# Performance work log

Measured on AMD Instinct MI355X. Metric: run time of the kernel, lower is better.

Reference implementation:

```python
import jax, jax.numpy as jnp
import numpy as np

# ---- static module config (matches init_kwargs) ----
N = 16384
E_DIM = 256
SHARE_N_E = 2048
SPECIFIC = [1024, 1024, 1024]
TOTAL_N_E = SHARE_N_E + sum(SPECIFIC)  # 5120
BETA = 0.25
NUM_MOD = len(SPECIFIC)
BIG = 1e7  # value written into masked-out distance entries

# prefix boundaries of the per-modality code blocks: [2048, 3072, 4096, 5120]
CODE_BOUNDS = jnp.asarray(np.cumsum([SHARE_N_E] + SPECIFIC)[:, None].squeeze(-1) if False else np.cumsum([SHARE_N_E] + SPECIFIC), dtype=jnp.int32)
# code -> modality id; shared codes get -1
CODE_MOD = jnp.searchsorted(CODE_BOUNDS, jnp.arange(TOTAL_N_E, dtype=jnp.int32), side='right') - 1  # [TOTAL_N_E]


def setup_inputs() -> dict:
    key = jax.random.key(0)
    k1, k2 = jax.random.split(key)
    x = jax.random.normal(k1, (N, E_DIM), dtype=jnp.float32)
    emb_weight = jax.random.normal(k2, (TOTAL_N_E, E_DIM), dtype=jnp.float32)  # nn.Embedding default N(0,1)
    split_index = jnp.array([0, 5120, 10240, 16384], dtype=jnp.int64)  # 3 equal modality segments
    return {"x": x, "emb_weight": emb_weight, "split_index": split_index}


def reference(x, emb_weight, split_index):
    # pairwise squared distances d[n, c] = ||x_n||^2 + ||e_c||^2 - 2 x_n . e_c
    d = (jnp.sum(x * x, axis=1, keepdims=True)
         + jnp.sum(emb_weight * emb_weight, axis=1)[None, :]
         - 2.0 * jnp.einsum('nd,cd->nc', x, emb_weight))  # [N, TOTAL_N_E]

    # token -> modality id via split boundaries (vectorized form of the Python loop)
    tok_mod = jnp.searchsorted(split_index, jnp.arange(N, dtype=split_index.dtype), side='right') - 1  # [N]
    tok_mod = tok_mod.astype(jnp.int32)
    # allowed = shared code OR code's modality matches token's modality
    allowed = (CODE_MOD[None, :] == -1) | (CODE_MOD[None, :] == tok_mod[:, None])  # [N, TOTAL_N_E]
    d = jnp.where(allowed, d, jnp.float32(BIG))

    indices = jnp.argmin(d, axis=-1)              # [N]
    x_q = jnp.take(emb_weight, indices, axis=0)   # [N, E_DIM]

    # per-modality VQ losses: codebook + beta * commitment (mse over segment)
    sg = jax.lax.stop_gradient
    se_commit = jnp.sum((sg(x_q) - x) ** 2, axis=1)   # [N]
    se_code = jnp.sum((x_q - sg(x)) ** 2, axis=1)     # [N]
    seg_commit = jax.ops.segment_sum(se_commit, tok_mod, num_segments=NUM_MOD)
    seg_code = jax.ops.segment_sum(se_code, tok_mod, num_segments=NUM_MOD)
    counts = (split_index[1:] - split_index[:-1]).astype(jnp.float32) * jnp.float32(E_DIM)
    q_losses = seg_code / counts + BETA * (seg_commit / counts)  # [NUM_MOD]

    # straight-through estimator
    x_q_ste = x + sg(x_q - x)
    return (x_q_ste, indices, d, q_losses)
```

## Files before the change

kernel.cpp:

```cpp
#include <hip/hip_runtime.h>
#include <stdint.h>

#define N_TOK    16384
#define E_DIM    256
#define N_CODE   5120
#define N_SHARED 2048
#define BIGF     1e7f

#define BM  128
#define BN  128
#define BK  32
#define NCB (N_CODE / BN)
#define NKC (E_DIM / BK)
#define CHUNK (BM * BK)

#define IDX_OFF ((size_t)N_TOK * E_DIM)
#define D_OFF   (IDX_OFF + N_TOK)
#define QL_OFF  (D_OFF + (size_t)N_TOK * N_CODE)

typedef float f32x4 __attribute__((ext_vector_type(4)));
typedef short bf16x8 __attribute__((ext_vector_type(8)));
typedef short s16x4 __attribute__((ext_vector_type(4)));

typedef __attribute__((address_space(1))) const unsigned int g_u32;
typedef __attribute__((address_space(3))) unsigned int lds_u32;

__device__ __forceinline__ unsigned short bf16_rn(float f) {
    unsigned u = __float_as_uint(f);
    u += 0x7FFF + ((u >> 16) & 1);
    return (unsigned short)(u >> 16);
}
__device__ __forceinline__ float bf16_to_f(unsigned short h) {
    return __uint_as_float(((unsigned)h) << 16);
}

__global__ __launch_bounds__(256) void convert_kernel(const float* __restrict__ x,
                                                      const float* __restrict__ emb,
                                                      float* __restrict__ xx,
                                                      float* __restrict__ ee,
                                                      short* __restrict__ xhi, short* __restrict__ xlo,
                                                      short* __restrict__ ehi, short* __restrict__ elo) {
    int wid = threadIdx.x >> 6, ln = threadIdx.x & 63;
    int row = blockIdx.x * 4 + wid;
    const float* src; float* nrm; short *hiA, *loA; int rl, tb;
    if (row < N_TOK) {
        src = x + (size_t)row * E_DIM; nrm = xx + row;
        tb = row >> 7; rl = row & 127; hiA = xhi; loA = xlo;
    } else {
        int r = row - N_TOK;
        src = emb + (size_t)r * E_DIM; nrm = ee + r;
        tb = r >> 7; rl = r & 127; hiA = ehi; loA = elo;
    }
    f32x4 v = ((const f32x4*)src)[ln];
    float s = v[0]*v[0] + v[1]*v[1] + v[2]*v[2] + v[3]*v[3];
    s16x4 h, l;
#pragma unroll
    for (int c = 0; c < 4; ++c) {
        unsigned short hh = bf16_rn(v[c]);
        h[c] = (short)hh;
        l[c] = (short)bf16_rn(v[c] - bf16_to_f(hh));
    }
    int kc = ln >> 3, q = (ln >> 1) & 3, kl4 = (ln & 1) * 4;
    size_t di = ((((size_t)tb * NKC + kc) * 4 + q) * BM + rl) * 8 + kl4;
    *(s16x4*)&hiA[di] = h;
    *(s16x4*)&loA[di] = l;
#pragma unroll
    for (int sh = 32; sh; sh >>= 1) s += __shfl_xor(s, sh, 64);
    if (ln == 0) *nrm = s;
}

__global__ __launch_bounds__(256, 2) void gemm_kernel(const short* __restrict__ xhi,
                                                      const short* __restrict__ xlo,
                                                      const short* __restrict__ ehi,
                                                      const short* __restrict__ elo,
                                                      const int* __restrict__ split,
                                                      const float* __restrict__ xx,
                                                      const float* __restrict__ ee,
                                                      float* __restrict__ out) {
    __shared__ short Ah[CHUNK], Al[CHUNK], Bh[CHUNK], Bl[CHUNK];
    __shared__ float xxs[BM];
    __shared__ float ees[BN];
    __shared__ float redv[2][BM];
    __shared__ int   redi[2][BM];

    const int bx = blockIdx.x;
    const int by = blockIdx.y;
    const int m0 = by * BM, n0 = bx * BN;
    const int t = threadIdx.x;

    const int s1 = split[1], s2v = split[2];
    const int tmFirst = (m0 >= s1) + (m0 >= s2v);
    const int tmLast  = ((m0 + BM - 1) >= s1) + ((m0 + BM - 1) >= s2v);
    const bool rowUni = (tmFirst == tmLast);
    const int cmod = (n0 < N_SHARED) ? -1 : ((n0 - N_SHARED) >> 10);

    float* dOut = out + D_OFF;
    float* pmin = out;
    int*   pidx = (int*)(out + (size_t)N_TOK * NCB);

    if (cmod >= 0 && rowUni && cmod != tmFirst) {
        int row = t >> 1, ch = t & 1;
        f32x4* p = (f32x4*)(dOut + (size_t)(m0 + row) * N_CODE + n0 + ch * 64);
        f32x4 big = {BIGF, BIGF, BIGF, BIGF};
#pragma unroll
        for (int u = 0; u < 16; ++u) p[u] = big;
        if (t < BM) {
            pmin[(size_t)(m0 + t) * NCB + bx] = BIGF;
            pidx[(size_t)(m0 + t) * NCB + bx] = n0;
        }
        return;
    }

    const bool allAllowed = (cmod < 0) || (rowUni && cmod == tmFirst);

    if (t < BM) xxs[t] = xx[m0 + t];
    else        ees[t - BM] = ee[n0 + (t - BM)];

    f32x4 acc[4][4] = {};

    const int wid = t >> 6, lane = t & 63;
    const int quad = lane >> 4, ln16 = lane & 15;
    const int wr = (wid >> 1) * 64, wc = (wid & 1) * 64;

    const short* aHiG = xhi + (size_t)by * NKC * CHUNK;
    const short* aLoG = xlo + (size_t)by * NKC * CHUNK;
    const short* bHiG = ehi + (size_t)bx * NKC * CHUNK;
    const short* bLoG = elo + (size_t)bx * NKC * CHUNK;
    const int tOff = t * 8;

    for (int kc = 0; kc < NKC; ++kc) {
        __syncthreads();
        const int co = kc * CHUNK;
#pragma unroll
        for (int p = 0; p < 2; ++p) {
            int o = p * 2048 + tOff;
            __builtin_amdgcn_global_load_lds((g_u32*)(aHiG + co + o), (lds_u32*)&Ah[o], 16, 0, 0);
            __builtin_amdgcn_global_load_lds((g_u32*)(aLoG + co + o), (lds_u32*)&Al[o], 16, 0, 0);
            __builtin_amdgcn_global_load_lds((g_u32*)(bHiG + co + o), (lds_u32*)&Bh[o], 16, 0, 0);
            __builtin_amdgcn_global_load_lds((g_u32*)(bLoG + co + o), (lds_u32*)&Bl[o], 16, 0, 0);
        }
        __syncthreads();

        bf16x8 ah[4], al[4], bh[4], bl[4];
#pragma unroll
        for (int i = 0; i < 4; ++i) {
            int a = (quad * BM + wr + i * 16 + ln16) * 8;
            ah[i] = *(const bf16x8*)&Ah[a];
            al[i] = *(const bf16x8*)&Al[a];
        }
#pragma unroll
        for (int j = 0; j < 4; ++j) {
            int b = (quad * BM + wc + j * 16 + ln16) * 8;
            bh[j] = *(const bf16x8*)&Bh[b];
            bl[j] = *(const bf16x8*)&Bl[b];
        }
#pragma unroll
        for (int i = 0; i < 4; ++i)
#pragma unroll
            for (int j = 0; j < 4; ++j) {
                acc[i][j] = __builtin_amdgcn_mfma_f32_16x16x32_bf16(ah[i], bh[j], acc[i][j], 0, 0, 0);
                acc[i][j] = __builtin_amdgcn_mfma_f32_16x16x32_bf16(ah[i], bl[j], acc[i][j], 0, 0, 0);
                acc[i][j] = __builtin_amdgcn_mfma_f32_16x16x32_bf16(al[i], bh[j], acc[i][j], 0, 0, 0);
            }
    }

#pragma unroll
    for (int i = 0; i < 4; ++i) {
#pragma unroll
        for (int r = 0; r < 4; ++r) {
            int lm = wr + i * 16 + quad * 4 + r;
            int gm = m0 + lm;
            float xv = xxs[lm];
            int tmod = (gm >= s1) + (gm >= s2v);
            float best = 3.4e38f;
            int bidx = n0;
#pragma unroll
            for (int j = 0; j < 4; ++j) {
                int lnn = wc + j * 16 + ln16;
                int gn = n0 + lnn;
                float dv = fmaf(-2.f, acc[i][j][r], xv + ees[lnn]);
                if (!allAllowed) {
                    bool ok = (gn < N_SHARED) || (((gn - N_SHARED) >> 10) == tmod);
                    if (!ok) dv = BIGF;
                }
                dOut[(size_t)gm * N_CODE + gn] = dv;
                if (dv < best) { best = dv; bidx = gn; }
            }
#pragma unroll
            for (int s = 1; s < 16; s <<= 1) {
                float ov = __shfl_xor(best, s, 64);
                int   oi = __shfl_xor(bidx, s, 64);
                if (ov < best || (ov == best && oi < bidx)) { best = ov; bidx = oi; }
            }
            if (ln16 == 0) { redv[wid & 1][lm] = best; redi[wid & 1][lm] = bidx; }
        }
    }
    __syncthreads();
    if (t < BM) {
        float v0 = redv[0][t]; int i0 = redi[0][t];
        float v1 = redv[1][t]; int i1 = redi[1][t];
        if (v1 < v0 || (v1 == v0 && i1 < i0)) { v0 = v1; i0 = i1; }
        pmin[(size_t)(m0 + t) * NCB + bx] = v0;
        pidx[(size_t)(m0 + t) * NCB + bx] = i0;
    }
}

__global__ __launch_bounds__(256) void reduce_kernel(float* __restrict__ out) {
    int tk = blockIdx.x * 256 + threadIdx.x;
    const float* pmin = out;
    const int* pidx = (const int*)(out + (size_t)N_TOK * NCB);
    float best = pmin[(size_t)tk * NCB];
    int bi = pidx[(size_t)tk * NCB];
    for (int j = 1; j < NCB; ++j) {
        float v = pmin[(size_t)tk * NCB + j];
        int ii = pidx[(size_t)tk * NCB + j];
        if (v < best || (v == best && ii < bi)) { best = v; bi = ii; }
    }
    out[IDX_OFF + tk] = (float)bi;
}

__global__ __launch_bounds__(256) void gather_kernel(const float* __restrict__ x,
                                                     const float* __restrict__ emb,
                                                     const int* __restrict__ split,
                                                     float* __restrict__ out,
                                                     float* __restrict__ wsLoss) {
    __shared__ float ls[3];
    int t = threadIdx.x, wid = t >> 6, ln = t & 63;
    if (t < 3) ls[t] = 0.f;
    __syncthreads();
    int tok = blockIdx.x * 4 + wid;
    int idx = (int)out[IDX_OFF + tok];
    f32x4 e  = ((const f32x4*)(emb + (size_t)idx * E_DIM))[ln];
    f32x4 xv = ((const f32x4*)(x + (size_t)tok * E_DIM))[ln];
    f32x4 q;
    float s = 0.f;
#pragma unroll
    for (int c = 0; c < 4; ++c) {
        float d = e[c] - xv[c];
        q[c] = xv[c] + d;
        s = fmaf(d, d, s);
    }
    ((f32x4*)(out + (size_t)tok * E_DIM))[ln] = q;
#pragma unroll
    for (int sh = 32; sh; sh >>= 1) s += __shfl_xor(s, sh, 64);
    if (ln == 0) {
        int mod = (tok >= split[1]) + (tok >= split[2]);
        atomicAdd(&ls[mod], s);
    }
    __syncthreads();
    if (t < 3) wsLoss[blockIdx.x * 3 + t] = ls[t];
}

__global__ __launch_bounds__(256) void loss_kernel(const float* __restrict__ wsLoss,
                                                   const int* __restrict__ split,
                                                   float* __restrict__ out, int nblk) {
    __shared__ float red[256];
    float s[3] = {0.f, 0.f, 0.f};
    for (int b = threadIdx.x; b < nblk; b += 256) {
        s[0] += wsLoss[b * 3 + 0];
        s[1] += wsLoss[b * 3 + 1];
        s[2] += wsLoss[b * 3 + 2];
    }
    for (int m = 0; m < 3; ++m) {
        red[threadIdx.x] = s[m];
        __syncthreads();
        for (int st = 128; st; st >>= 1) {
            if (threadIdx.x < st) red[threadIdx.x] += red[threadIdx.x + st];
            __syncthreads();
        }
        if (threadIdx.x == 0) {
            float cnt = (float)(split[m + 1] - split[m]) * (float)E_DIM;
            float a = red[0] / cnt;
            out[QL_OFF + m] = a + 0.25f * a;
        }
        __syncthreads();
    }
}

extern "C" void kernel_launch(void* const* d_in, const int* in_sizes, int n_in,
                              void* d_out, int out_size, void* d_ws, size_t ws_size,
                              hipStream_t stream) {
    const float* x   = (const float*)d_in[0];
    const float* emb = (const float*)d_in[1];
    const int* split = (const int*)d_in[2];
    float* out = (float*)d_out;

    float* xx     = (float*)d_ws;
    float* ee     = xx + N_TOK;
    float* wsLoss = ee + N_CODE;
    short* xhi    = (short*)(wsLoss + 4096 * 3);
    short* xlo    = xhi + (size_t)N_TOK * E_DIM;
    short* ehi    = xlo + (size_t)N_TOK * E_DIM;
    short* elo    = ehi + (size_t)N_CODE * E_DIM;
    int nblkGather = N_TOK / 4;

    convert_kernel<<<dim3((N_TOK + N_CODE) / 4), dim3(256), 0, stream>>>(x, emb, xx, ee, xhi, xlo, ehi, elo);
    gemm_kernel<<<dim3(NCB, N_TOK / BM), dim3(256), 0, stream>>>(xhi, xlo, ehi, elo, split, xx, ee, out);
    reduce_kernel<<<dim3(N_TOK / 256), dim3(256), 0, stream>>>(out);
    gather_kernel<<<dim3(nblkGather), dim3(256), 0, stream>>>(x, emb, split, out, wsLoss);
    loss_kernel<<<dim3(1), dim3(256), 0, stream>>>(wsLoss, split, out, nblkGather);
}
```

Measured before the change: 485.6 us.

## Enlarge GEMM tiles to 256x256, double-buffer LDS, fuse argmin reduce into gather

Raises the distance GEMM tile from 128x128 to 256x256 with 512 threads and double-buffered LDS. Loads of the hi and lo bf16 halves are split into staggered stages with explicit vmcnt waits and raised MFMA priority, so global-to-LDS transfers overlap the three-pass split-bf16 MFMA. The partial argmin arrays move to workspace, and the standalone reduce kernel is folded into the gather kernel as a wave shuffle reduction. The costs are higher register pressure (32 accumulators per thread), more LDS use that may cut occupancy, and fewer blocks in the grid.

```diff
diff --git a/kernel.cpp b/kernel.cpp
--- a/kernel.cpp
+++ b/kernel.cpp
@@ -7,11 +7,11 @@
 #define N_SHARED 2048
 #define BIGF     1e7f
 
-#define BM  128
-#define BN  128
+#define BM  256
+#define BN  256
 #define BK  32
 #define NCB (N_CODE / BN)
-#define NKC (E_DIM / BK)
+#define NKT (E_DIM / BK)
 #define CHUNK (BM * BK)
 
 #define IDX_OFF ((size_t)N_TOK * E_DIM)
@@ -24,6 +24,8 @@
 
 typedef __attribute__((address_space(1))) const unsigned int g_u32;
 typedef __attribute__((address_space(3))) unsigned int lds_u32;
+
+#define VMW(n) asm volatile("s_waitcnt vmcnt(" #n ")" ::: "memory")
 
 __device__ __forceinline__ unsigned short bf16_rn(float f) {
     unsigned u = __float_as_uint(f);
@@ -45,11 +47,11 @@
     const float* src; float* nrm; short *hiA, *loA; int rl, tb;
     if (row < N_TOK) {
         src = x + (size_t)row * E_DIM; nrm = xx + row;
-        tb = row >> 7; rl = row & 127; hiA = xhi; loA = xlo;
+        tb = row >> 8; rl = row & 255; hiA = xhi; loA = xlo;
     } else {
         int r = row - N_TOK;
         src = emb + (size_t)r * E_DIM; nrm = ee + r;
-        tb = r >> 7; rl = r & 127; hiA = ehi; loA = elo;
+        tb = r >> 8; rl = r & 255; hiA = ehi; loA = elo;
     }
     f32x4 v = ((const f32x4*)src)[ln];
     float s = v[0]*v[0] + v[1]*v[1] + v[2]*v[2] + v[3]*v[3];
@@ -60,8 +62,8 @@
         h[c] = (short)hh;
         l[c] = (short)bf16_rn(v[c] - bf16_to_f(hh));
     }
-    int kc = ln >> 3, q = (ln >> 1) & 3, kl4 = (ln & 1) * 4;
-    size_t di = ((((size_t)tb * NKC + kc) * 4 + q) * BM + rl) * 8 + kl4;
+    int kt = ln >> 3, q = (ln >> 1) & 3, kl4 = (ln & 1) * 4;
+    size_t di = ((((size_t)tb * NKT + kt) * 4 + q) * BM + rl) * 8 + kl4;
     *(s16x4*)&hiA[di] = h;
     *(s16x4*)&loA[di] = l;
 #pragma unroll
@@ -69,19 +71,22 @@
     if (ln == 0) *nrm = s;
 }
 
-__global__ __launch_bounds__(256, 2) void gemm_kernel(const short* __restrict__ xhi,
+__global__ __launch_bounds__(512, 2) void gemm_kernel(const short* __restrict__ xhi,
                                                       const short* __restrict__ xlo,
                                                       const short* __restrict__ ehi,
                                                       const short* __restrict__ elo,
                                                       const int* __restrict__ split,
                                                       const float* __restrict__ xx,
                                                       const float* __restrict__ ee,
-                                                      float* __restrict__ out) {
-    __shared__ short Ah[CHUNK], Al[CHUNK], Bh[CHUNK], Bl[CHUNK];
+                                                      float* __restrict__ out,
+                                                      float* __restrict__ pmin,
+                                                      int*   __restrict__ pidx) {
+    __shared__ short Ah[2][CHUNK], Bh[2][CHUNK];
+    __shared__ short Al[2][CHUNK], Bl[2][CHUNK];
     __shared__ float xxs[BM];
     __shared__ float ees[BN];
-    __shared__ float redv[2][BM];
-    __shared__ int   redi[2][BM];
+    __shared__ float redv[4][BM];
+    __shared__ int   redi[4][BM];
 
     const int bx = blockIdx.x;
     const int by = blockIdx.y;
@@ -95,15 +100,13 @@
     const int cmod = (n0 < N_SHARED) ? -1 : ((n0 - N_SHARED) >> 10);
 
     float* dOut = out + D_OFF;
-    float* pmin = out;
-    int*   pidx = (int*)(out + (size_t)N_TOK * NCB);
 
     if (cmod >= 0 && rowUni && cmod != tmFirst) {
-        int row = t >> 1, ch = t & 1;
-        f32x4* p = (f32x4*)(dOut + (size_t)(m0 + row) * N_CODE + n0 + ch * 64);
+        int row = t >> 1, half = t & 1;
+        f32x4* p = (f32x4*)(dOut + (size_t)(m0 + row) * N_CODE + n0 + half * 128);
         f32x4 big = {BIGF, BIGF, BIGF, BIGF};
 #pragma unroll
-        for (int u = 0; u < 16; ++u) p[u] = big;
+        for (int u = 0; u < 32; ++u) p[u] = big;
         if (t < BM) {
             pmin[(size_t)(m0 + t) * NCB + bx] = BIGF;
             pidx[(size_t)(m0 + t) * NCB + bx] = n0;
@@ -115,57 +118,88 @@
 
     if (t < BM) xxs[t] = xx[m0 + t];
     else        ees[t - BM] = ee[n0 + (t - BM)];
-
-    f32x4 acc[4][4] = {};
+    __syncthreads();
+
+    f32x4 acc[8][4] = {};
 
     const int wid = t >> 6, lane = t & 63;
     const int quad = lane >> 4, ln16 = lane & 15;
-    const int wr = (wid >> 1) * 64, wc = (wid & 1) * 64;
-
-    const short* aHiG = xhi + (size_t)by * NKC * CHUNK;
-    const short* aLoG = xlo + (size_t)by * NKC * CHUNK;
-    const short* bHiG = ehi + (size_t)bx * NKC * CHUNK;
-    const short* bLoG = elo + (size_t)bx * NKC * CHUNK;
+    const int wr = (wid >> 2) * 128, wc = (wid & 3) * 64;
+    const int qb = quad * BM;
+
+    const short* aHiG = xhi + (size_t)by * NKT * CHUNK;
+    const short* aLoG = xlo + (size_t)by * NKT * CHUNK;
+    const short* bHiG = ehi + (size_t)bx * NKT * CHUNK;
+    const short* bLoG = elo + (size_t)bx * NKT * CHUNK;
     const int tOff = t * 8;
 
-    for (int kc = 0; kc < NKC; ++kc) {
-        __syncthreads();
-        const int co = kc * CHUNK;
+    auto stageU0 = [&](int kt, int b) {
+        const size_t co = (size_t)kt * CHUNK;
 #pragma unroll
         for (int p = 0; p < 2; ++p) {
-            int o = p * 2048 + tOff;
-            __builtin_amdgcn_global_load_lds((g_u32*)(aHiG + co + o), (lds_u32*)&Ah[o], 16, 0, 0);
-            __builtin_amdgcn_global_load_lds((g_u32*)(aLoG + co + o), (lds_u32*)&Al[o], 16, 0, 0);
-            __builtin_amdgcn_global_load_lds((g_u32*)(bHiG + co + o), (lds_u32*)&Bh[o], 16, 0, 0);
-            __builtin_amdgcn_global_load_lds((g_u32*)(bLoG + co + o), (lds_u32*)&Bl[o], 16, 0, 0);
-        }
-        __syncthreads();
-
-        bf16x8 ah[4], al[4], bh[4], bl[4];
-#pragma unroll
-        for (int i = 0; i < 4; ++i) {
-            int a = (quad * BM + wr + i * 16 + ln16) * 8;
-            ah[i] = *(const bf16x8*)&Ah[a];
-            al[i] = *(const bf16x8*)&Al[a];
-        }
-#pragma unroll
-        for (int j = 0; j < 4; ++j) {
-            int b = (quad * BM + wc + j * 16 + ln16) * 8;
-            bh[j] = *(const bf16x8*)&Bh[b];
-            bl[j] = *(const bf16x8*)&Bl[b];
-        }
-#pragma unroll
-        for (int i = 0; i < 4; ++i)
-#pragma unroll
-            for (int j = 0; j < 4; ++j) {
-                acc[i][j] = __builtin_amdgcn_mfma_f32_16x16x32_bf16(ah[i], bh[j], acc[i][j], 0, 0, 0);
-                acc[i][j] = __builtin_amdgcn_mfma_f32_16x16x32_bf16(ah[i], bl[j], acc[i][j], 0, 0, 0);
-                acc[i][j] = __builtin_amdgcn_mfma_f32_16x16x32_bf16(al[i], bh[j], acc[i][j], 0, 0, 0);
-            }
-    }
-
-#pragma unroll
-    for (int i = 0; i < 4; ++i) {
+            int o = p * 4096 + tOff;
+            __builtin_amdgcn_global_load_lds((g_u32*)(aHiG + co + o), (lds_u32*)&Ah[b][o], 16, 0, 0);
+            __builtin_amdgcn_global_load_lds((g_u32*)(bHiG + co + o), (lds_u32*)&Bh[b][o], 16, 0, 0);
+        }
+    };
+    auto stageU1 = [&](int kt, int b) {
+        const size_t co = (size_t)kt * CHUNK;
+#pragma unroll
+        for (int p = 0; p < 2; ++p) {
+            int o = p * 4096 + tOff;
+            __builtin_amdgcn_global_load_lds((g_u32*)(aLoG + co + o), (lds_u32*)&Al[b][o], 16, 0, 0);
+            __builtin_amdgcn_global_load_lds((g_u32*)(bLoG + co + o), (lds_u32*)&Bl[b][o], 16, 0, 0);
+        }
+    };
+
+    stageU0(0, 0); stageU1(0, 0); stageU0(1, 1);
+    int cur = 0;
+
+#define TILE(VA, VB, DOU1, DOU2, KT)                                                         \
+    {                                                                                        \
+        VMW(VA);                                                                             \
+        __builtin_amdgcn_s_barrier();                                                        \
+        if (DOU1) stageU1((KT) + 1, cur ^ 1);                                                \
+        bf16x8 ah[8], bh[4];                                                                 \
+        _Pragma("unroll") for (int i = 0; i < 8; ++i)                                        \
+            ah[i] = *(const bf16x8*)&Ah[cur][(qb + wr + i * 16 + ln16) * 8];                 \
+        _Pragma("unroll") for (int j = 0; j < 4; ++j)                                        \
+            bh[j] = *(const bf16x8*)&Bh[cur][(qb + wc + j * 16 + ln16) * 8];                 \
+        __builtin_amdgcn_s_setprio(1);                                                       \
+        _Pragma("unroll") for (int i = 0; i < 8; ++i)                                        \
+            _Pragma("unroll") for (int j = 0; j < 4; ++j)                                    \
+                acc[i][j] = __builtin_amdgcn_mfma_f32_16x16x32_bf16(ah[i], bh[j], acc[i][j], 0, 0, 0); \
+        __builtin_amdgcn_s_setprio(0);                                                       \
+        VMW(VB);                                                                             \
+        __builtin_amdgcn_s_barrier();                                                        \
+        if (DOU2) stageU0((KT) + 2, cur);                                                    \
+        bf16x8 bl[4];                                                                        \
+        _Pragma("unroll") for (int j = 0; j < 4; ++j)                                        \
+            bl[j] = *(const bf16x8*)&Bl[cur][(qb + wc + j * 16 + ln16) * 8];                 \
+        __builtin_amdgcn_s_setprio(1);                                                       \
+        _Pragma("unroll") for (int i = 0; i < 8; ++i)                                        \
+            _Pragma("unroll") for (int j = 0; j < 4; ++j)                                    \
+                acc[i][j] = __builtin_amdgcn_mfma_f32_16x16x32_bf16(ah[i], bl[j], acc[i][j], 0, 0, 0); \
+        __builtin_amdgcn_s_setprio(0);                                                       \
+        bf16x8 al[8];                                                                        \
+        _Pragma("unroll") for (int i = 0; i < 8; ++i)                                        \
+            al[i] = *(const bf16x8*)&Al[cur][(qb + wr + i * 16 + ln16) * 8];                 \
+        __builtin_amdgcn_s_setprio(1);                                                       \
+        _Pragma("unroll") for (int i = 0; i < 8; ++i)                                        \
+            _Pragma("unroll") for (int j = 0; j < 4; ++j)                                    \
+                acc[i][j] = __builtin_amdgcn_mfma_f32_16x16x32_bf16(al[i], bh[j], acc[i][j], 0, 0, 0); \
+        __builtin_amdgcn_s_setprio(0);                                                       \
+        cur ^= 1;                                                                            \
+    }
+
+    for (int kt = 0; kt < NKT - 2; ++kt)
+        TILE(8, 8, true, true, kt);
+    TILE(8, 8, true, false, NKT - 2);
+    TILE(4, 0, false, false, NKT - 1);
+#undef TILE
+
+#pragma unroll
+    for (int i = 0; i < 8; ++i) {
 #pragma unroll
         for (int r = 0; r < 4; ++r) {
             int lm = wr + i * 16 + quad * 4 + r;
@@ -192,44 +226,50 @@
                 int   oi = __shfl_xor(bidx, s, 64);
                 if (ov < best || (ov == best && oi < bidx)) { best = ov; bidx = oi; }
             }
-            if (ln16 == 0) { redv[wid & 1][lm] = best; redi[wid & 1][lm] = bidx; }
+            if (ln16 == 0) { redv[wid & 3][lm] = best; redi[wid & 3][lm] = bidx; }
         }
     }
     __syncthreads();
     if (t < BM) {
         float v0 = redv[0][t]; int i0 = redi[0][t];
-        float v1 = redv[1][t]; int i1 = redi[1][t];
-        if (v1 < v0 || (v1 == v0 && i1 < i0)) { v0 = v1; i0 = i1; }
+#pragma unroll
+        for (int w = 1; w < 4; ++w) {
+            float v = redv[w][t]; int ii = redi[w][t];
+            if (v < v0 || (v == v0 && ii < i0)) { v0 = v; i0 = ii; }
+        }
         pmin[(size_t)(m0 + t) * NCB + bx] = v0;
         pidx[(size_t)(m0 + t) * NCB + bx] = i0;
     }
-}
-
-__global__ __launch_bounds__(256) void reduce_kernel(float* __restrict__ out) {
-    int tk = blockIdx.x * 256 + threadIdx.x;
-    const float* pmin = out;
-    const int* pidx = (const int*)(out + (size_t)N_TOK * NCB);
-    float best = pmin[(size_t)tk * NCB];
-    int bi = pidx[(size_t)tk * NCB];
-    for (int j = 1; j < NCB; ++j) {
-        float v = pmin[(size_t)tk * NCB + j];
-        int ii = pidx[(size_t)tk * NCB + j];
-        if (v < best || (v == best && ii < bi)) { best = v; bi = ii; }
-    }
-    out[IDX_OFF + tk] = (float)bi;
 }
 
 __global__ __launch_bounds__(256) void gather_kernel(const float* __restrict__ x,
                                                      const float* __restrict__ emb,
                                                      const int* __restrict__ split,
                                                      float* __restrict__ out,
+                                                     const float* __restrict__ pmin,
+                                                     const int* __restrict__ pidx,
                                                      float* __restrict__ wsLoss) {
     __shared__ float ls[3];
     int t = threadIdx.x, wid = t >> 6, ln = t & 63;
     if (t < 3) ls[t] = 0.f;
     __syncthreads();
     int tok = blockIdx.x * 4 + wid;
-    int idx = (int)out[IDX_OFF + tok];
+
+    float best = 3.4e38f;
+    int bi = 0x7fffffff;
+    if (ln < NCB) {
+        best = pmin[(size_t)tok * NCB + ln];
+        bi   = pidx[(size_t)tok * NCB + ln];
+    }
+#pragma unroll
+    for (int sh = 32; sh; sh >>= 1) {
+        float ov = __shfl_xor(best, sh, 64);
+        int   oi = __shfl_xor(bi, sh, 64);
+        if (ov < best || (ov == best && oi < bi)) { best = ov; bi = oi; }
+    }
+    if (ln == 0) out[IDX_OFF + tok] = (float)bi;
+    int idx = bi;
+
     f32x4 e  = ((const f32x4*)(emb + (size_t)idx * E_DIM))[ln];
     f32x4 xv = ((const f32x4*)(x + (size_t)tok * E_DIM))[ln];
     f32x4 q;
@@ -288,15 +328,16 @@
     float* xx     = (float*)d_ws;
     float* ee     = xx + N_TOK;
     float* wsLoss = ee + N_CODE;
-    short* xhi    = (short*)(wsLoss + 4096 * 3);
+    float* pmin   = wsLoss + 4096 * 3;
+    int*   pidx   = (int*)(pmin + (size_t)N_TOK * NCB);
+    short* xhi    = (short*)(pidx + (size_t)N_TOK * NCB);
     short* xlo    = xhi + (size_t)N_TOK * E_DIM;
     short* ehi    = xlo + (size_t)N_TOK * E_DIM;
     short* elo    = ehi + (size_t)N_CODE * E_DIM;
     int nblkGather = N_TOK / 4;
 
     convert_kernel<<<dim3((N_TOK + N_CODE) / 4), dim3(256), 0, stream>>>(x, emb, xx, ee, xhi, xlo, ehi, elo);
-    gemm_kernel<<<dim3(NCB, N_TOK / BM), dim3(256), 0, stream>>>(xhi, xlo, ehi, elo, split, xx, ee, out);
-    reduce_kernel<<<dim3(N_TOK / 256), dim3(256), 0, stream>>>(out);
-    gather_kernel<<<dim3(nblkGather), dim3(256), 0, stream>>>(x, emb, split, out, wsLoss);
+    gemm_kernel<<<dim3(NCB, N_TOK / BM), dim3(512), 0, stream>>>(xhi, xlo, ehi, elo, split, xx, ee, out, pmin, pidx);
+    gather_kernel<<<dim3(nblkGather), dim3(256), 0, stream>>>(x, emb, split, out, pmin, pidx, wsLoss);
     loss_kernel<<<dim3(1), dim3(256), 0, stream>>>(wsLoss, split, out, nblkGather);
 }
```

Measured after the change: 498.6 us. +2.7%, slower.
